# Performance work log

Hardware: AMD Instinct MI355X
Metric: run time of the kernel (lower is better)

The kernel has to match this reference:

```python
import jax, jax.numpy as jnp
import numpy as np

B, T, D, HS = 8, 2048, 768, 64
H = D // HS  # 12 heads
LN_EPS = 1e-5


def setup_inputs() -> dict:
    key = jax.random.key(0)
    ks = jax.random.split(key, 8)
    s = 0.02
    x = jax.random.normal(ks[0], (B, T, D), jnp.float32)
    Wx = jax.random.normal(ks[1], (D, D), jnp.float32) * s
    Ww = jax.random.normal(ks[2], (D, D), jnp.float32) * 0.01  # w_proj.weight ~ N(0,0.01)
    # w_proj bias schedule: logit(1 - linspace(0.9,0.999,H)) per head, expanded over head_size
    r_sched = jnp.linspace(0.9, 0.999, H)
    w_target = 1.0 - r_sched
    bw = jnp.log(w_target / (1.0 - w_target))          # logit
    bw = jnp.repeat(bw[:, None], HS, axis=1).reshape(-1)  # (D,)
    Wk = jax.random.normal(ks[3], (D, D), jnp.float32) * s
    Wv = jax.random.normal(ks[4], (D, D), jnp.float32) * s
    Wr = jax.random.normal(ks[5], (D, D), jnp.float32) * s
    Wo = jax.random.normal(ks[6], (D, D), jnp.float32) * s
    gamma = jnp.ones((D,), jnp.float32)
    beta = jnp.zeros((D,), jnp.float32)
    return {"x": x, "Wx": Wx, "Ww": Ww, "bw": bw, "Wk": Wk, "Wv": Wv,
            "Wr": Wr, "Wo": Wo, "gamma": gamma, "beta": beta}


def _layernorm(x, gamma, beta):
    mu = jnp.mean(x, axis=-1, keepdims=True)
    var = jnp.mean(jnp.square(x - mu), axis=-1, keepdims=True)
    return (x - mu) * jax.lax.rsqrt(var + LN_EPS) * gamma + beta


def _selective_scan(k, v, w):
    """k,v,w: (T,B,H,HS). State S: (B,H,HS,HS).
    S_t = (1 - w_t) * S_{t-1} (decay along key dim) + k_t (x) v_t;  y_t = k_t . S_t."""
    S0 = jnp.zeros((B, H, HS, HS), k.dtype)

    def step(S, inp):
        kt, vt, wt = inp  # each (B,H,HS)
        S = S * (1.0 - wt)[..., :, None] + kt[..., :, None] * vt[..., None, :]
        yt = jnp.einsum('bhi,bhij->bhj', kt, S)
        return S, yt

    _, ys = jax.lax.scan(step, S0, (k, v, w))
    return ys  # (T,B,H,HS)


def reference(x, Wx, Ww, bw, Wk, Wv, Wr, Wo, gamma, beta):
    xn = _layernorm(x, gamma, beta)                       # (B,T,D)
    xp = jnp.einsum('btd,ed->bte', xn, Wx)                # x_proj
    w = jax.nn.sigmoid(jnp.einsum('bte,fe->btf', xp, Ww) + bw)
    k = jnp.einsum('btd,ed->bte', xn, Wk)
    v = jnp.einsum('btd,ed->bte', xn, Wv)
    r = jax.nn.sigmoid(jnp.einsum('btd,ed->bte', xn, Wr))

    def to_scan(a):  # (B,T,D) -> (T,B,H,HS)
        return a.reshape(B, T, H, HS).transpose(1, 0, 2, 3)

    ys = _selective_scan(to_scan(k), to_scan(v), to_scan(w))  # (T,B,H,HS)
    y = ys.transpose(1, 0, 2, 3).reshape(B, T, D)
    y = y * r
    return jnp.einsum('btd,ed->bte', y, Wo)
```

## Files before the change

kernel.cpp:

```cpp
#include <hip/hip_runtime.h>

#define B_ 8
#define T_ 2048
#define D_ 768
#define H_ 12
#define HS_ 64
#define LN_EPS 1e-5f
#define NC 32
#define TC 64
#define PA 72
#define PV 68

typedef __attribute__((ext_vector_type(8))) short bf16x8;
typedef __attribute__((ext_vector_type(4))) float f32x4;

__device__ __forceinline__ ushort f2bf(float f) {
  unsigned u = __builtin_bit_cast(unsigned, f);
  unsigned r = (u + 0x7FFFu + ((u >> 16) & 1u)) >> 16;
  return (ushort)r;
}
__device__ __forceinline__ float bf2f(ushort u) {
  return __builtin_bit_cast(float, ((unsigned)u) << 16);
}

__device__ __forceinline__ bf16x8 ldsT68(const ushort* tile, int r0, int col) {
  bf16x8 r;
#pragma unroll
  for (int e = 0; e < 8; ++e) r[e] = (short)tile[(r0 + e) * PV + col];
  return r;
}

__global__ __launch_bounds__(256) void zero_out_kernel(float* __restrict__ out, int n) {
  for (int i = blockIdx.x * 256 + threadIdx.x; i < n; i += gridDim.x * 256)
    out[i] = 0.f;
}

__global__ __launch_bounds__(256) void cast_w_kernel(
    const float* __restrict__ src, ushort* __restrict__ dst) {
  int idx = (blockIdx.x * 256 + threadIdx.x) * 4;
  float4 v = *reinterpret_cast<const float4*>(src + idx);
  ushort4 o;
  o.x = f2bf(v.x); o.y = f2bf(v.y); o.z = f2bf(v.z); o.w = f2bf(v.w);
  *reinterpret_cast<ushort4*>(dst + idx) = o;
}

__global__ __launch_bounds__(256) void ln_kernel(
    const float* __restrict__ x, const float* __restrict__ gamma,
    const float* __restrict__ beta, ushort* __restrict__ xn) {
  const int wv = threadIdx.x >> 6;
  const int lane = threadIdx.x & 63;
  const int row = blockIdx.x * 4 + wv;
  const float* xr = x + (size_t)row * D_;
  float4 a[3];
#pragma unroll
  for (int s = 0; s < 3; ++s)
    a[s] = *reinterpret_cast<const float4*>(xr + s * 256 + lane * 4);
  float sum = 0.f;
#pragma unroll
  for (int s = 0; s < 3; ++s) sum += a[s].x + a[s].y + a[s].z + a[s].w;
#pragma unroll
  for (int off = 32; off; off >>= 1) sum += __shfl_xor(sum, off);
  float mu = sum * (1.f / 768.f);
  float vs = 0.f;
#pragma unroll
  for (int s = 0; s < 3; ++s) {
    float dx = a[s].x - mu, dy = a[s].y - mu, dz = a[s].z - mu, dw = a[s].w - mu;
    vs += dx * dx + dy * dy + dz * dz + dw * dw;
  }
#pragma unroll
  for (int off = 32; off; off >>= 1) vs += __shfl_xor(vs, off);
  float rs = rsqrtf(vs * (1.f / 768.f) + LN_EPS);
  ushort* orow = xn + (size_t)row * D_;
#pragma unroll
  for (int s = 0; s < 3; ++s) {
    int col = s * 256 + lane * 4;
    float4 g = *reinterpret_cast<const float4*>(gamma + col);
    float4 bb = *reinterpret_cast<const float4*>(beta + col);
    ushort4 o;
    o.x = f2bf((a[s].x - mu) * rs * g.x + bb.x);
    o.y = f2bf((a[s].y - mu) * rs * g.y + bb.y);
    o.z = f2bf((a[s].z - mu) * rs * g.z + bb.z);
    o.w = f2bf((a[s].w - mu) * rs * g.w + bb.w);
    *reinterpret_cast<ushort4*>(orow + col) = o;
  }
}

__global__ __launch_bounds__(512, 2) void gemm256(
    const ushort* __restrict__ A, const ushort* __restrict__ W,
    float* __restrict__ Cf,
    ushort* __restrict__ d0, ushort* __restrict__ d1,
    ushort* __restrict__ d2, ushort* __restrict__ d3,
    const float* __restrict__ bias, int mode) {
  __shared__ __align__(16) ushort lds[65536];
  const int tid = threadIdx.x;
  const int wid = tid >> 6;
  const int lane = tid & 63;
  const int wr = wid >> 2, wc = wid & 3;
  const int fr = lane & 15, fq = lane >> 4;
  const int m0 = blockIdx.x * 256, n0 = blockIdx.y * 256;
  const int strow = tid >> 3;
  const int stblk = tid & 7;

  const int RA0 = wr * 8192;
  const int RA1 = 32768 + wr * 8192;
  const int RB0 = 16384 + (wc >> 1) * 8192 + (wc & 1) * 4096;
  const int RB1 = 49152 + (wc >> 1) * 8192 + (wc & 1) * 4096;

  f32x4 acc[8][4];
#pragma unroll
  for (int m = 0; m < 8; ++m)
#pragma unroll
    for (int n = 0; n < 4; ++n) acc[m][n] = (f32x4){0.f, 0.f, 0.f, 0.f};

#define STAGE_HALF(gb, grow0, kk0, roff)                                          \
  {                                                                               \
    _Pragma("unroll") for (int j = 0; j < 2; ++j) {                               \
      const int lr_ = j * 64 + strow;                                             \
      const int bs_ = stblk ^ (lr_ & 7);                                          \
      const ushort* s_ = (gb) + (size_t)((grow0) + lr_) * 768 + (kk0) + bs_ * 8;  \
      __builtin_amdgcn_global_load_lds(                                           \
          (const __attribute__((address_space(1))) void*)s_,                      \
          (__attribute__((address_space(3))) void*)(lds + (roff) + j * 4096 + wid * 512), \
          16, 0, 0);                                                              \
    }                                                                             \
  }

#define LDF(dst, base, rf, kk)                                                    \
  dst = *reinterpret_cast<const bf16x8*>(                                         \
      lds + (base) + ((rf)*16 + fr) * 64 + ((((kk)*4 + fq) ^ (fr & 7)) * 8));

#define MFMA_Q(mb, nb, aa, bb)                                                    \
  __builtin_amdgcn_s_setprio(1);                                                  \
  _Pragma("unroll") for (int m_ = 0; m_ < 4; ++m_)                                \
  _Pragma("unroll") for (int n_ = 0; n_ < 2; ++n_)                                \
  _Pragma("unroll") for (int k_ = 0; k_ < 2; ++k_)                                \
    acc[(mb) + m_][(nb) + n_] = __builtin_amdgcn_mfma_f32_16x16x32_bf16(          \
        aa[m_][k_], bb[n_][k_], acc[(mb) + m_][(nb) + n_], 0, 0, 0);              \
  __builtin_amdgcn_s_setprio(0);

  STAGE_HALF(A, m0, 0, 0);
  STAGE_HALF(A, m0 + 128, 0, 8192);
  STAGE_HALF(W, n0, 0, 16384);
  STAGE_HALF(W, n0 + 128, 0, 24576);
  STAGE_HALF(W, n0, 64, 49152);
  STAGE_HALF(W, n0 + 128, 64, 57344);
  asm volatile("s_waitcnt vmcnt(4)" ::: "memory");
  __builtin_amdgcn_s_barrier();

  bf16x8 aL[4][2], aH[4][2], bL[2][2], bH[2][2];

  for (int i = 0; i < 6; ++i) {
    const int kQ = (2 * i + 1) * 64;
    const int kP2 = (2 * i + 2 <= 11 ? 2 * i + 2 : 11) * 64;
    const int kQ2 = (2 * i + 3 <= 11 ? 2 * i + 3 : 11) * 64;

    STAGE_HALF(A, m0, kQ, 32768);
#pragma unroll
    for (int m = 0; m < 4; ++m) { LDF(aL[m][0], RA0, m, 0); LDF(aL[m][1], RA0, m, 1); }
#pragma unroll
    for (int n = 0; n < 2; ++n) { LDF(bL[n][0], RB0, n, 0); LDF(bL[n][1], RB0, n, 1); }
    __builtin_amdgcn_s_barrier();
    MFMA_Q(0, 0, aL, bL);
    __builtin_amdgcn_s_barrier();
    STAGE_HALF(A, m0 + 128, kQ, 40960);
#pragma unroll
    for (int n = 0; n < 2; ++n) { LDF(bH[n][0], RB0, n + 2, 0); LDF(bH[n][1], RB0, n + 2, 1); }
    __builtin_amdgcn_s_barrier();
    MFMA_Q(0, 2, aL, bH);
    __builtin_amdgcn_s_barrier();
    STAGE_HALF(W, n0, kP2, 16384);
#pragma unroll
    for (int m = 0; m < 4; ++m) { LDF(aH[m][0], RA0, m + 4, 0); LDF(aH[m][1], RA0, m + 4, 1); }
    __builtin_amdgcn_s_barrier();
    MFMA_Q(4, 0, aH, bL);
    __builtin_amdgcn_s_barrier();
    STAGE_HALF(W, n0 + 128, kP2, 24576);
    __builtin_amdgcn_s_barrier();
    MFMA_Q(4, 2, aH, bH);
    asm volatile("s_waitcnt vmcnt(4)" ::: "memory");
    __builtin_amdgcn_s_barrier();

    STAGE_HALF(A, m0, kP2, 0);
#pragma unroll
    for (int m = 0; m < 4; ++m) { LDF(aL[m][0], RA1, m, 0); LDF(aL[m][1], RA1, m, 1); }
#pragma unroll
    for (int n = 0; n < 2; ++n) { LDF(bL[n][0], RB1, n, 0); LDF(bL[n][1], RB1, n, 1); }
    __builtin_amdgcn_s_barrier();
    MFMA_Q(0, 0, aL, bL);
    __builtin_amdgcn_s_barrier();
    STAGE_HALF(A, m0 + 128, kP2, 8192);
#pragma unroll
    for (int n = 0; n < 2; ++n) { LDF(bH[n][0], RB1, n + 2, 0); LDF(bH[n][1], RB1, n + 2, 1); }
    __builtin_amdgcn_s_barrier();
    MFMA_Q(0, 2, aL, bH);
    __builtin_amdgcn_s_barrier();
    STAGE_HALF(W, n0, kQ2, 49152);
#pragma unroll
    for (int m = 0; m < 4; ++m) { LDF(aH[m][0], RA1, m + 4, 0); LDF(aH[m][1], RA1, m + 4, 1); }
    __builtin_amdgcn_s_barrier();
    MFMA_Q(4, 0, aH, bL);
    __builtin_amdgcn_s_barrier();
    STAGE_HALF(W, n0 + 128, kQ2, 57344);
    __builtin_amdgcn_s_barrier();
    MFMA_Q(4, 2, aH, bH);
    asm volatile("s_waitcnt vmcnt(4)" ::: "memory");
    __builtin_amdgcn_s_barrier();
  }

  const int r0 = fq * 4;
  if (mode == 5) {
    const int sel = n0 >= 2304 ? 3 : n0 >= 1536 ? 2 : n0 >= 768 ? 1 : 0;
    ushort* dst = sel == 0 ? d0 : sel == 1 ? d1 : sel == 2 ? d2 : d3;
    const int nb = n0 - sel * 768;
    const bool sig = (sel == 2);
#pragma unroll
    for (int mf = 0; mf < 8; ++mf)
#pragma unroll
      for (int nf = 0; nf < 4; ++nf) {
        int gr = m0 + wr * 128 + mf * 16 + r0;
        int gc = nb + wc * 64 + nf * 16 + fr;
#pragma unroll
        for (int rr = 0; rr < 4; ++rr) {
          float v = acc[mf][nf][rr];
          if (sig) v = 1.f / (1.f + __expf(-v));
          dst[(size_t)(gr + rr) * 768 + gc] = f2bf(v);
        }
      }
  } else if (mode == 3) {
#pragma unroll
    for (int mf = 0; mf < 8; ++mf)
#pragma unroll
      for (int nf = 0; nf < 4; ++nf) {
        int gr = m0 + wr * 128 + mf * 16 + r0;
        int gc = n0 + wc * 64 + nf * 16 + fr;
        float bv = bias[gc];
#pragma unroll
        for (int rr = 0; rr < 4; ++rr) {
          float u = acc[mf][nf][rr] + bv;
          Cf[(size_t)(gr + rr) * 768 + gc] = 1.f / (1.f + __expf(u));
        }
      }
  } else {
#pragma unroll
    for (int mf = 0; mf < 8; ++mf)
#pragma unroll
      for (int nf = 0; nf < 4; ++nf) {
        int gr = m0 + wr * 128 + mf * 16 + r0;
        int gc = n0 + wc * 64 + nf * 16 + fr;
#pragma unroll
        for (int rr = 0; rr < 4; ++rr)
          Cf[(size_t)(gr + rr) * 768 + gc] = acc[mf][nf][rr];
      }
  }
#undef STAGE_HALF
#undef LDF
#undef MFMA_Q
}

__global__ __launch_bounds__(64) void scan_prep(
    const ushort* __restrict__ kb, const float* __restrict__ dg,
    ushort* __restrict__ kA, ushort* __restrict__ kIA, float* __restrict__ aend) {
  const int bh = blockIdx.x, c = blockIdx.y;
  const int b = bh / H_, h = bh % H_;
  const int i = threadIdx.x;
  size_t go = (size_t)b * T_ * D_ + (size_t)(c * TC) * D_ + h * HS_ + i;
  size_t co = ((size_t)bh * T_ + (size_t)c * TC) * HS_ + i;
  float a = 1.f;
#pragma unroll 4
  for (int t = 0; t < TC; ++t) {
    float d = dg[go];
    float k = bf2f(kb[go]);
    a *= d;
    kA[co] = f2bf(k * a);
    kIA[co] = f2bf(k / a);
    go += D_;
    co += HS_;
  }
  aend[((size_t)bh * NC + c) * HS_ + i] = a;
}

__global__ __launch_bounds__(256) void scan_mc(
    const ushort* __restrict__ kIA, const ushort* __restrict__ vb,
    char* __restrict__ McBase) {
  __shared__ __align__(16) ushort kt[TC * PV];
  __shared__ __align__(16) ushort vt[TC * PV];
  const int bh = blockIdx.x, c = blockIdx.y;
  const int b = bh / H_, h = bh % H_;
  const int tid = threadIdx.x;
  const int w = tid >> 6, lane = tid & 63;
  const int fr = lane & 15, fq = lane >> 4;
  {
    const int row = tid >> 2, col = (tid & 3) * 16;
    const ushort* gki = kIA + ((size_t)bh * T_ + (size_t)c * TC + row) * HS_ + col;
    const ushort* gv = vb + ((size_t)b * T_ + (size_t)c * TC + row) * D_ + h * HS_ + col;
    uint4 i0 = *(const uint4*)gki; uint4 i1 = *(const uint4*)(gki + 8);
    uint4 v0 = *(const uint4*)gv;  uint4 v1 = *(const uint4*)(gv + 8);
    ushort* pk = kt + row * PV + col;
    *(uint2*)(pk + 0) = make_uint2(i0.x, i0.y);
    *(uint2*)(pk + 4) = make_uint2(i0.z, i0.w);
    *(uint2*)(pk + 8) = make_uint2(i1.x, i1.y);
    *(uint2*)(pk + 12) = make_uint2(i1.z, i1.w);
    ushort* pv = vt + row * PV + col;
    *(uint2*)(pv + 0) = make_uint2(v0.x, v0.y);
    *(uint2*)(pv + 4) = make_uint2(v0.z, v0.w);
    *(uint2*)(pv + 8) = make_uint2(v1.x, v1.y);
    *(uint2*)(pv + 12) = make_uint2(v1.z, v1.w);
  }
  __syncthreads();
  f32x4 zero = {0.f, 0.f, 0.f, 0.f};
  f32x4 acc[4] = {zero, zero, zero, zero};
#pragma unroll
  for (int kk = 0; kk < 2; ++kk) {
    bf16x8 af = ldsT68(kt, kk * 32 + fq * 8, w * 16 + fr);
#pragma unroll
    for (int nf = 0; nf < 4; ++nf) {
      bf16x8 b8 = ldsT68(vt, kk * 32 + fq * 8, nf * 16 + fr);
      acc[nf] = __builtin_amdgcn_mfma_f32_16x16x32_bf16(af, b8, acc[nf], 0, 0, 0);
    }
  }
  float* mc = (float*)(McBase + ((size_t)bh * NC + c) * 16384);
#pragma unroll
  for (int nf = 0; nf < 4; ++nf)
#pragma unroll
    for (int rr = 0; rr < 4; ++rr) {
      int i = w * 16 + fq * 4 + rr, j = nf * 16 + fr;
      mc[i * 64 + j] = acc[nf][rr];
    }
}

__global__ __launch_bounds__(256) void scan_chain(
    char* __restrict__ McBase, const float* __restrict__ aend) {
  const int bh = blockIdx.x;
  const int i = threadIdx.x >> 2, j0 = (threadIdx.x & 3) * 16;
  float S[16];
#pragma unroll
  for (int p = 0; p < 16; ++p) S[p] = 0.f;
  for (int c = 0; c < NC; ++c) {
    char* slot = McBase + ((size_t)bh * NC + c) * 16384;
    const float* mc = (const float*)slot + i * 64 + j0;
    float m[16];
#pragma unroll
    for (int p = 0; p < 16; ++p) m[p] = mc[p];
    __syncthreads();
    ushort* s0 = (ushort*)slot + i * 64 + j0;
#pragma unroll
    for (int p = 0; p < 16; ++p) s0[p] = f2bf(S[p]);
    float ae = aend[((size_t)bh * NC + c) * HS_ + i];
#pragma unroll
    for (int p = 0; p < 16; ++p) S[p] = ae * (S[p] + m[p]);
  }
}

__global__ __launch_bounds__(256) void scan_y(
    const ushort* __restrict__ kA, const ushort* __restrict__ kIA,
    const ushort* __restrict__ vb, const ushort* __restrict__ rb,
    const char* __restrict__ McBase, ushort* __restrict__ yrow) {
  __shared__ __align__(16) ushort kAt[TC * PA];
  __shared__ __align__(16) ushort kIAt[TC * PA];
  __shared__ __align__(16) ushort Vt[TC * PV];
  __shared__ __align__(16) ushort S0t[TC * PV];
  __shared__ __align__(16) ushort Am[TC * PA];
  const int bh = blockIdx.x, c = blockIdx.y;
  const int b = bh / H_, h = bh % H_;
  const int tid = threadIdx.x;
  const int w = tid >> 6, lane = tid & 63;
  const int fr = lane & 15, fq = lane >> 4;
  {
    const int row = tid >> 2, col = (tid & 3) * 16;
    const ushort* gka = kA + ((size_t)bh * T_ + (size_t)c * TC + row) * HS_ + col;
    const ushort* gki = kIA + ((size_t)bh * T_ + (size_t)c * TC + row) * HS_ + col;
    const ushort* gv = vb + ((size_t)b * T_ + (size_t)c * TC + row) * D_ + h * HS_ + col;
    const ushort* gs = (const ushort*)(McBase + ((size_t)bh * NC + c) * 16384) + row * HS_ + col;
    uint4 a0 = *(const uint4*)gka; uint4 a1 = *(const uint4*)(gka + 8);
    uint4 i0 = *(const uint4*)gki; uint4 i1 = *(const uint4*)(gki + 8);
    uint4 v0 = *(const uint4*)gv;  uint4 v1 = *(const uint4*)(gv + 8);
    uint4 s0 = *(const uint4*)gs;  uint4 s1 = *(const uint4*)(gs + 8);
    *(uint4*)&kAt[row * PA + col] = a0;
    *(uint4*)&kAt[row * PA + col + 8] = a1;
    *(uint4*)&kIAt[row * PA + col] = i0;
    *(uint4*)&kIAt[row * PA + col + 8] = i1;
    ushort* pv = Vt + row * PV + col;
    *(uint2*)(pv + 0) = make_uint2(v0.x, v0.y);
    *(uint2*)(pv + 4) = make_uint2(v0.z, v0.w);
    *(uint2*)(pv + 8) = make_uint2(v1.x, v1.y);
    *(uint2*)(pv + 12) = make_uint2(v1.z, v1.w);
    ushort* ps = S0t + row * PV + col;
    *(uint2*)(ps + 0) = make_uint2(s0.x, s0.y);
    *(uint2*)(ps + 4) = make_uint2(s0.z, s0.w);
    *(uint2*)(ps + 8) = make_uint2(s1.x, s1.y);
    *(uint2*)(ps + 12) = make_uint2(s1.z, s1.w);
  }
  __syncthreads();

  f32x4 zero = {0.f, 0.f, 0.f, 0.f};
  {
    f32x4 accA[4] = {zero, zero, zero, zero};
#pragma unroll
    for (int kk = 0; kk < 2; ++kk) {
      bf16x8 af = *reinterpret_cast<const bf16x8*>(&kAt[(w * 16 + fr) * PA + kk * 32 + fq * 8]);
#pragma unroll
      for (int nf = 0; nf < 4; ++nf) {
        bf16x8 b8 = *reinterpret_cast<const bf16x8*>(&kIAt[(nf * 16 + fr) * PA + kk * 32 + fq * 8]);
        accA[nf] = __builtin_amdgcn_mfma_f32_16x16x32_bf16(af, b8, accA[nf], 0, 0, 0);
      }
    }
#pragma unroll
    for (int nf = 0; nf < 4; ++nf)
#pragma unroll
      for (int rr = 0; rr < 4; ++rr) {
        int t = w * 16 + fq * 4 + rr;
        int s = nf * 16 + fr;
        float val = (s <= t) ? accA[nf][rr] : 0.f;
        Am[t * PA + s] = f2bf(val);
      }
  }
  __syncthreads();

  f32x4 accY[4] = {zero, zero, zero, zero};
#pragma unroll
  for (int kk = 0; kk < 2; ++kk) {
    bf16x8 af = *reinterpret_cast<const bf16x8*>(&kAt[(w * 16 + fr) * PA + kk * 32 + fq * 8]);
#pragma unroll
    for (int nf = 0; nf < 4; ++nf) {
      bf16x8 b8 = ldsT68(S0t, kk * 32 + fq * 8, nf * 16 + fr);
      accY[nf] = __builtin_amdgcn_mfma_f32_16x16x32_bf16(af, b8, accY[nf], 0, 0, 0);
    }
  }
#pragma unroll
  for (int kk = 0; kk < 2; ++kk) {
    bf16x8 af = *reinterpret_cast<const bf16x8*>(&Am[(w * 16 + fr) * PA + kk * 32 + fq * 8]);
#pragma unroll
    for (int nf = 0; nf < 4; ++nf) {
      bf16x8 b8 = ldsT68(Vt, kk * 32 + fq * 8, nf * 16 + fr);
      accY[nf] = __builtin_amdgcn_mfma_f32_16x16x32_bf16(af, b8, accY[nf], 0, 0, 0);
    }
  }
#pragma unroll
  for (int nf = 0; nf < 4; ++nf)
#pragma unroll
    for (int rr = 0; rr < 4; ++rr) {
      int t = w * 16 + fq * 4 + rr;
      int j = nf * 16 + fr;
      size_t go = ((size_t)b * T_ + (size_t)c * TC + t) * D_ + h * HS_ + j;
      float rv = bf2f(rb[go]);
      yrow[go] = f2bf(accY[nf][rr] * rv);
    }
}

extern "C" void kernel_launch(void* const* d_in, const int* in_sizes, int n_in,
                              void* d_out, int out_size, void* d_ws, size_t ws_size,
                              hipStream_t stream) {
  const float* x     = (const float*)d_in[0];
  const float* Wx    = (const float*)d_in[1];
  const float* Ww    = (const float*)d_in[2];
  const float* bw    = (const float*)d_in[3];
  const float* Wk    = (const float*)d_in[4];
  const float* Wv    = (const float*)d_in[5];
  const float* Wr    = (const float*)d_in[6];
  const float* Wo    = (const float*)d_in[7];
  const float* gamma = (const float*)d_in[8];
  const float* beta  = (const float*)d_in[9];
  float* out = (float*)d_out;

  const size_t NEED = 208404480ull;
  if (ws_size < NEED) {
    zero_out_kernel<<<2048, 256, 0, stream>>>(out, out_size);
    return;
  }

  char* ws = (char*)d_ws;
  ushort* xn = (ushort*)ws;
  ushort* wb = (ushort*)(ws + 25165824);
  ushort* xp = (ushort*)(ws + 32243712);
  ushort* kb = (ushort*)(ws + 57409536);
  ushort* vb = (ushort*)(ws + 82575360);
  ushort* rb = (ushort*)(ws + 107741184);
  ushort* yr = (ushort*)(ws + 132907008);
  float*  df = (float*)(ws + 158072832);
  ushort* kAb  = (ushort*)ws;
  ushort* kIAb = (ushort*)(ws + 32243712);
  float*  aendb = (float*)(ws + 132907008);
  char*   McBase = (char*)(ws + 158072832);

  ushort* WcatB = wb;
  ushort* WwB = wb + 4 * 589824;
  ushort* WoB = wb + 5 * 589824;

  cast_w_kernel<<<576, 256, 0, stream>>>(Wk, WcatB);
  cast_w_kernel<<<576, 256, 0, stream>>>(Wv, WcatB + 589824);
  cast_w_kernel<<<576, 256, 0, stream>>>(Wr, WcatB + 2 * 589824);
  cast_w_kernel<<<576, 256, 0, stream>>>(Wx, WcatB + 3 * 589824);
  cast_w_kernel<<<576, 256, 0, stream>>>(Ww, WwB);
  cast_w_kernel<<<576, 256, 0, stream>>>(Wo, WoB);
  ln_kernel<<<4096, 256, 0, stream>>>(x, gamma, beta, xn);

  gemm256<<<dim3(64, 12), 512, 0, stream>>>(xn, WcatB, nullptr, kb, vb, rb, xp,
                                            nullptr, 5);
  gemm256<<<dim3(64, 3), 512, 0, stream>>>(xp, WwB, df, nullptr, nullptr, nullptr,
                                           nullptr, bw, 3);

  scan_prep<<<dim3(96, NC), 64, 0, stream>>>(kb, df, kAb, kIAb, aendb);
  scan_mc<<<dim3(96, NC), 256, 0, stream>>>(kIAb, vb, McBase);
  scan_chain<<<96, 256, 0, stream>>>(McBase, aendb);
  scan_y<<<dim3(96, NC), 256, 0, stream>>>(kAb, kIAb, vb, rb, McBase, yr);

  gemm256<<<dim3(64, 3), 512, 0, stream>>>(yr, WoB, out, nullptr, nullptr, nullptr,
                                           nullptr, nullptr, 0);
}
```

Measured before the change: 277.6 us.

## Fuse scan prep into chunk kernels, store V in MFMA fragment layout, pipeline GEMM LDS

```diff
diff --git a/kernel.cpp b/kernel.cpp
--- a/kernel.cpp
+++ b/kernel.cpp
@@ -8,8 +8,6 @@
 #define LN_EPS 1e-5f
 #define NC 32
 #define TC 64
-#define PA 72
-#define PV 68
 
 typedef __attribute__((ext_vector_type(8))) short bf16x8;
 typedef __attribute__((ext_vector_type(4))) float f32x4;
@@ -23,11 +21,11 @@
   return __builtin_bit_cast(float, ((unsigned)u) << 16);
 }
 
-__device__ __forceinline__ bf16x8 ldsT68(const ushort* tile, int r0, int col) {
-  bf16x8 r;
-#pragma unroll
-  for (int e = 0; e < 8; ++e) r[e] = (short)tile[(r0 + e) * PV + col];
-  return r;
+__device__ __forceinline__ int fragaddr(int t, int i) {
+  return ((t >> 4) * 2 + (i >> 5)) * 512 + ((((i >> 3) & 3) * 16) + (t & 15)) * 8 + (i & 7);
+}
+__device__ __forceinline__ int fragswz(int i) {
+  return (((i >> 3) & 3) << 3) ^ (((i >> 5) & 1) << 5);
 }
 
 __global__ __launch_bounds__(256) void zero_out_kernel(float* __restrict__ out, int n) {
@@ -138,6 +136,15 @@
         aa[m_][k_], bb[n_][k_], acc[(mb) + m_][(nb) + n_], 0, 0, 0);              \
   __builtin_amdgcn_s_setprio(0);
 
+#define LDF_AL(RA) \
+  _Pragma("unroll") for (int m = 0; m < 4; ++m) { LDF(aL[m][0], RA, m, 0); LDF(aL[m][1], RA, m, 1); }
+#define LDF_AH(RA) \
+  _Pragma("unroll") for (int m = 0; m < 4; ++m) { LDF(aH[m][0], RA, m + 4, 0); LDF(aH[m][1], RA, m + 4, 1); }
+#define LDF_BL(RB) \
+  _Pragma("unroll") for (int n = 0; n < 2; ++n) { LDF(bL[n][0], RB, n, 0); LDF(bL[n][1], RB, n, 1); }
+#define LDF_BH(RB) \
+  _Pragma("unroll") for (int n = 0; n < 2; ++n) { LDF(bH[n][0], RB, n + 2, 0); LDF(bH[n][1], RB, n + 2, 1); }
+
   STAGE_HALF(A, m0, 0, 0);
   STAGE_HALF(A, m0 + 128, 0, 8192);
   STAGE_HALF(W, n0, 0, 16384);
@@ -148,6 +155,8 @@
   __builtin_amdgcn_s_barrier();
 
   bf16x8 aL[4][2], aH[4][2], bL[2][2], bH[2][2];
+  LDF_AL(RA0);
+  LDF_BL(RB0);
 
   for (int i = 0; i < 6; ++i) {
     const int kQ = (2 * i + 1) * 64;
@@ -155,77 +164,95 @@
     const int kQ2 = (2 * i + 3 <= 11 ? 2 * i + 3 : 11) * 64;
 
     STAGE_HALF(A, m0, kQ, 32768);
-#pragma unroll
-    for (int m = 0; m < 4; ++m) { LDF(aL[m][0], RA0, m, 0); LDF(aL[m][1], RA0, m, 1); }
-#pragma unroll
-    for (int n = 0; n < 2; ++n) { LDF(bL[n][0], RB0, n, 0); LDF(bL[n][1], RB0, n, 1); }
+    LDF_BH(RB0);
     __builtin_amdgcn_s_barrier();
     MFMA_Q(0, 0, aL, bL);
     __builtin_amdgcn_s_barrier();
+
     STAGE_HALF(A, m0 + 128, kQ, 40960);
-#pragma unroll
-    for (int n = 0; n < 2; ++n) { LDF(bH[n][0], RB0, n + 2, 0); LDF(bH[n][1], RB0, n + 2, 1); }
+    LDF_AH(RA0);
     __builtin_amdgcn_s_barrier();
     MFMA_Q(0, 2, aL, bH);
     __builtin_amdgcn_s_barrier();
+
     STAGE_HALF(W, n0, kP2, 16384);
-#pragma unroll
-    for (int m = 0; m < 4; ++m) { LDF(aH[m][0], RA0, m + 4, 0); LDF(aH[m][1], RA0, m + 4, 1); }
     __builtin_amdgcn_s_barrier();
     MFMA_Q(4, 0, aH, bL);
     __builtin_amdgcn_s_barrier();
+
     STAGE_HALF(W, n0 + 128, kP2, 24576);
-    __builtin_amdgcn_s_barrier();
+    asm volatile("s_waitcnt vmcnt(4)" ::: "memory");
+    __builtin_amdgcn_s_barrier();
+    LDF_AL(RA1);
+    LDF_BL(RB1);
     MFMA_Q(4, 2, aH, bH);
+    __builtin_amdgcn_s_barrier();
+
+    STAGE_HALF(A, m0, kP2, 0);
+    LDF_BH(RB1);
+    __builtin_amdgcn_s_barrier();
+    MFMA_Q(0, 0, aL, bL);
+    __builtin_amdgcn_s_barrier();
+
+    STAGE_HALF(A, m0 + 128, kP2, 8192);
+    LDF_AH(RA1);
+    __builtin_amdgcn_s_barrier();
+    MFMA_Q(0, 2, aL, bH);
+    __builtin_amdgcn_s_barrier();
+
+    STAGE_HALF(W, n0, kQ2, 49152);
+    __builtin_amdgcn_s_barrier();
+    MFMA_Q(4, 0, aH, bL);
+    __builtin_amdgcn_s_barrier();
+
+    STAGE_HALF(W, n0 + 128, kQ2, 57344);
     asm volatile("s_waitcnt vmcnt(4)" ::: "memory");
     __builtin_amdgcn_s_barrier();
-
-    STAGE_HALF(A, m0, kP2, 0);
-#pragma unroll
-    for (int m = 0; m < 4; ++m) { LDF(aL[m][0], RA1, m, 0); LDF(aL[m][1], RA1, m, 1); }
-#pragma unroll
-    for (int n = 0; n < 2; ++n) { LDF(bL[n][0], RB1, n, 0); LDF(bL[n][1], RB1, n, 1); }
-    __builtin_amdgcn_s_barrier();
-    MFMA_Q(0, 0, aL, bL);
-    __builtin_amdgcn_s_barrier();
-    STAGE_HALF(A, m0 + 128, kP2, 8192);
-#pragma unroll
-    for (int n = 0; n < 2; ++n) { LDF(bH[n][0], RB1, n + 2, 0); LDF(bH[n][1], RB1, n + 2, 1); }
-    __builtin_amdgcn_s_barrier();
-    MFMA_Q(0, 2, aL, bH);
-    __builtin_amdgcn_s_barrier();
-    STAGE_HALF(W, n0, kQ2, 49152);
-#pragma unroll
-    for (int m = 0; m < 4; ++m) { LDF(aH[m][0], RA1, m + 4, 0); LDF(aH[m][1], RA1, m + 4, 1); }
-    __builtin_amdgcn_s_barrier();
-    MFMA_Q(4, 0, aH, bL);
-    __builtin_amdgcn_s_barrier();
-    STAGE_HALF(W, n0 + 128, kQ2, 57344);
-    __builtin_amdgcn_s_barrier();
+    LDF_AL(RA0);
+    LDF_BL(RB0);
     MFMA_Q(4, 2, aH, bH);
-    asm volatile("s_waitcnt vmcnt(4)" ::: "memory");
     __builtin_amdgcn_s_barrier();
   }
 
   const int r0 = fq * 4;
   if (mode == 5) {
     const int sel = n0 >= 2304 ? 3 : n0 >= 1536 ? 2 : n0 >= 768 ? 1 : 0;
-    ushort* dst = sel == 0 ? d0 : sel == 1 ? d1 : sel == 2 ? d2 : d3;
     const int nb = n0 - sel * 768;
-    const bool sig = (sel == 2);
-#pragma unroll
-    for (int mf = 0; mf < 8; ++mf)
-#pragma unroll
-      for (int nf = 0; nf < 4; ++nf) {
-        int gr = m0 + wr * 128 + mf * 16 + r0;
-        int gc = nb + wc * 64 + nf * 16 + fr;
-#pragma unroll
-        for (int rr = 0; rr < 4; ++rr) {
-          float v = acc[mf][nf][rr];
-          if (sig) v = 1.f / (1.f + __expf(-v));
-          dst[(size_t)(gr + rr) * 768 + gc] = f2bf(v);
+    if (sel == 1) {
+#pragma unroll
+      for (int mf = 0; mf < 8; ++mf)
+#pragma unroll
+        for (int nf = 0; nf < 4; ++nf) {
+          int gr = m0 + wr * 128 + mf * 16 + r0;
+          int gc = nb + wc * 64 + nf * 16 + fr;
+          int b = gr >> 11, t = gr & 2047;
+          int c = t >> 6, s0 = t & 63;
+          int h = gc >> 6, j = gc & 63;
+          size_t addr = ((size_t)((b * 12 + h) * 32 + c)) * 4096 +
+                        (size_t)(((j >> 4) * 2 + (s0 >> 5)) * 512 +
+                                 (((s0 >> 3) & 3) * 16 + (j & 15)) * 8 + (s0 & 7));
+          ushort4 o;
+          o.x = f2bf(acc[mf][nf][0]); o.y = f2bf(acc[mf][nf][1]);
+          o.z = f2bf(acc[mf][nf][2]); o.w = f2bf(acc[mf][nf][3]);
+          *reinterpret_cast<ushort4*>(d1 + addr) = o;
         }
-      }
+    } else {
+      ushort* dst = sel == 0 ? d0 : sel == 2 ? d2 : d3;
+      const bool sig = (sel == 2);
+#pragma unroll
+      for (int mf = 0; mf < 8; ++mf)
+#pragma unroll
+        for (int nf = 0; nf < 4; ++nf) {
+          int gr = m0 + wr * 128 + mf * 16 + r0;
+          int gc = nb + wc * 64 + nf * 16 + fr;
+#pragma unroll
+          for (int rr = 0; rr < 4; ++rr) {
+            float v = acc[mf][nf][rr];
+            if (sig) v = 1.f / (1.f + __expf(-v));
+            dst[(size_t)(gr + rr) * 768 + gc] = f2bf(v);
+          }
+        }
+    }
   } else if (mode == 3) {
 #pragma unroll
     for (int mf = 0; mf < 8; ++mf)
@@ -255,155 +282,183 @@
 #undef STAGE_HALF
 #undef LDF
 #undef MFMA_Q
-}
-
-__global__ __launch_bounds__(64) void scan_prep(
-    const ushort* __restrict__ kb, const float* __restrict__ dg,
-    ushort* __restrict__ kA, ushort* __restrict__ kIA, float* __restrict__ aend) {
+#undef LDF_AL
+#undef LDF_AH
+#undef LDF_BL
+#undef LDF_BH
+}
+
+__global__ __launch_bounds__(256) void scan_mc2(
+    const ushort* __restrict__ kb, const float* __restrict__ df,
+    const ushort* __restrict__ vbF, ushort* __restrict__ McT,
+    float* __restrict__ aend) {
+  __shared__ float dt[64 * 68];
+  __shared__ ushort kt[64 * 72];
+  __shared__ ushort kIAf[4096];
+  __shared__ float part[256];
   const int bh = blockIdx.x, c = blockIdx.y;
   const int b = bh / H_, h = bh % H_;
-  const int i = threadIdx.x;
-  size_t go = (size_t)b * T_ * D_ + (size_t)(c * TC) * D_ + h * HS_ + i;
-  size_t co = ((size_t)bh * T_ + (size_t)c * TC) * HS_ + i;
+  const int tid = threadIdx.x;
+  const int w = tid >> 6, lane = tid & 63;
+  {
+    const int row = tid >> 2, c16 = (tid & 3) * 16;
+    const ushort* gk = kb + ((size_t)(b * T_ + c * TC + row)) * D_ + h * HS_ + c16;
+    const float* gd = df + ((size_t)(b * T_ + c * TC + row)) * D_ + h * HS_ + c16;
+    uint4 k0 = *(const uint4*)gk;
+    uint4 k1 = *(const uint4*)(gk + 8);
+    *(uint4*)&kt[row * 72 + c16] = k0;
+    *(uint4*)&kt[row * 72 + c16 + 8] = k1;
+#pragma unroll
+    for (int q = 0; q < 4; ++q)
+      *(float4*)&dt[row * 68 + c16 + q * 4] = *(const float4*)(gd + q * 4);
+  }
+  __syncthreads();
+  float p = 1.f;
+#pragma unroll
+  for (int tt = 0; tt < 16; ++tt) p *= dt[(w * 16 + tt) * 68 + lane];
+  part[w * 64 + lane] = p;
+  __syncthreads();
   float a = 1.f;
-#pragma unroll 4
-  for (int t = 0; t < TC; ++t) {
-    float d = dg[go];
-    float k = bf2f(kb[go]);
+  for (int w2 = 0; w2 < w; ++w2) a *= part[w2 * 64 + lane];
+#pragma unroll
+  for (int tt = 0; tt < 16; ++tt) {
+    int t = w * 16 + tt;
+    float d = dt[t * 68 + lane];
+    float k = bf2f(kt[t * 72 + lane]);
     a *= d;
-    kA[co] = f2bf(k * a);
-    kIA[co] = f2bf(k / a);
-    go += D_;
-    co += HS_;
-  }
-  aend[((size_t)bh * NC + c) * HS_ + i] = a;
-}
-
-__global__ __launch_bounds__(256) void scan_mc(
-    const ushort* __restrict__ kIA, const ushort* __restrict__ vb,
-    char* __restrict__ McBase) {
-  __shared__ __align__(16) ushort kt[TC * PV];
-  __shared__ __align__(16) ushort vt[TC * PV];
+    kIAf[fragaddr(lane, t)] = f2bf(k / a);
+  }
+  if (w == 3) aend[((size_t)bh * NC + c) * 64 + lane] = a;
+  __syncthreads();
+
+  const int fr = lane & 15, fq = lane >> 4;
+  f32x4 acc[4];
+#pragma unroll
+  for (int nf = 0; nf < 4; ++nf) acc[nf] = (f32x4){0.f, 0.f, 0.f, 0.f};
+  bf16x8 af[2];
+  af[0] = *reinterpret_cast<const bf16x8*>(&kIAf[(w * 2 + 0) * 512 + lane * 8]);
+  af[1] = *reinterpret_cast<const bf16x8*>(&kIAf[(w * 2 + 1) * 512 + lane * 8]);
+  const ushort* vch = vbF + ((size_t)bh * NC + c) * 4096;
+#pragma unroll
+  for (int kk = 0; kk < 2; ++kk)
+#pragma unroll
+    for (int nf = 0; nf < 4; ++nf) {
+      bf16x8 b8 = *reinterpret_cast<const bf16x8*>(vch + (nf * 2 + kk) * 512 + lane * 8);
+      acc[nf] = __builtin_amdgcn_mfma_f32_16x16x32_bf16(af[kk], b8, acc[nf], 0, 0, 0);
+    }
+  ushort* mch = McT + ((size_t)bh * NC + c) * 4096;
+#pragma unroll
+  for (int nf = 0; nf < 4; ++nf) {
+    ushort4 o;
+    o.x = f2bf(acc[nf][0]); o.y = f2bf(acc[nf][1]);
+    o.z = f2bf(acc[nf][2]); o.w = f2bf(acc[nf][3]);
+    *reinterpret_cast<ushort4*>(&mch[(nf * 16 + fr) * 64 + w * 16 + fq * 4]) = o;
+  }
+}
+
+__global__ __launch_bounds__(256) void scan_chain2(
+    const ushort* __restrict__ McT, const float* __restrict__ aend,
+    ushort* __restrict__ S0F) {
+  const int bh = blockIdx.x;
+  const int j = threadIdx.x >> 2, i0 = (threadIdx.x & 3) * 16;
+  const int fbase = ((j >> 4) * 2 + (i0 >> 5)) * 512 + (((i0 >> 3) & 3) * 16 + (j & 15)) * 8;
+  float S[16];
+#pragma unroll
+  for (int p = 0; p < 16; ++p) S[p] = 0.f;
+  for (int c = 0; c < NC; ++c) {
+    const ushort* mch = McT + ((size_t)bh * NC + c) * 4096 + j * 64 + i0;
+    bf16x8 m0 = *reinterpret_cast<const bf16x8*>(mch);
+    bf16x8 m1 = *reinterpret_cast<const bf16x8*>(mch + 8);
+    const float* ae = aend + ((size_t)bh * NC + c) * 64 + i0;
+    float av[16];
+#pragma unroll
+    for (int q = 0; q < 4; ++q) {
+      float4 aq = *(const float4*)(ae + q * 4);
+      av[q * 4 + 0] = aq.x; av[q * 4 + 1] = aq.y; av[q * 4 + 2] = aq.z; av[q * 4 + 3] = aq.w;
+    }
+    ushort* s0 = S0F + ((size_t)bh * NC + c) * 4096 + fbase;
+    ushort4 o0, o1, o2, o3;
+    o0.x = f2bf(S[0]); o0.y = f2bf(S[1]); o0.z = f2bf(S[2]); o0.w = f2bf(S[3]);
+    o1.x = f2bf(S[4]); o1.y = f2bf(S[5]); o1.z = f2bf(S[6]); o1.w = f2bf(S[7]);
+    o2.x = f2bf(S[8]); o2.y = f2bf(S[9]); o2.z = f2bf(S[10]); o2.w = f2bf(S[11]);
+    o3.x = f2bf(S[12]); o3.y = f2bf(S[13]); o3.z = f2bf(S[14]); o3.w = f2bf(S[15]);
+    *reinterpret_cast<ushort4*>(s0) = o0;
+    *reinterpret_cast<ushort4*>(s0 + 4) = o1;
+    *reinterpret_cast<ushort4*>(s0 + 128) = o2;
+    *reinterpret_cast<ushort4*>(s0 + 132) = o3;
+#pragma unroll
+    for (int p = 0; p < 8; ++p) S[p] = av[p] * (S[p] + bf2f((ushort)m0[p]));
+#pragma unroll
+    for (int p = 0; p < 8; ++p) S[8 + p] = av[8 + p] * (S[8 + p] + bf2f((ushort)m1[p]));
+  }
+}
+
+__global__ __launch_bounds__(256) void scan_y2(
+    const ushort* __restrict__ kb, const float* __restrict__ df,
+    const ushort* __restrict__ vbF, const ushort* __restrict__ rb,
+    const ushort* __restrict__ S0F, ushort* __restrict__ yrow) {
+  __shared__ float dt[64 * 68];
+  __shared__ ushort kt[64 * 72];
+  __shared__ ushort kAf[4096];
+  __shared__ ushort kIAf[4096];
+  __shared__ ushort Am[64 * 72];
+  __shared__ float part[256];
   const int bh = blockIdx.x, c = blockIdx.y;
   const int b = bh / H_, h = bh % H_;
   const int tid = threadIdx.x;
   const int w = tid >> 6, lane = tid & 63;
   const int fr = lane & 15, fq = lane >> 4;
   {
-    const int row = tid >> 2, col = (tid & 3) * 16;
-    const ushort* gki = kIA + ((size_t)bh * T_ + (size_t)c * TC + row) * HS_ + col;
-    const ushort* gv = vb + ((size_t)b * T_ + (size_t)c * TC + row) * D_ + h * HS_ + col;
-    uint4 i0 = *(const uint4*)gki; uint4 i1 = *(const uint4*)(gki + 8);
-    uint4 v0 = *(const uint4*)gv;  uint4 v1 = *(const uint4*)(gv + 8);
-    ushort* pk = kt + row * PV + col;
-    *(uint2*)(pk + 0) = make_uint2(i0.x, i0.y);
-    *(uint2*)(pk + 4) = make_uint2(i0.z, i0.w);
-    *(uint2*)(pk + 8) = make_uint2(i1.x, i1.y);
-    *(uint2*)(pk + 12) = make_uint2(i1.z, i1.w);
-    ushort* pv = vt + row * PV + col;
-    *(uint2*)(pv + 0) = make_uint2(v0.x, v0.y);
-    *(uint2*)(pv + 4) = make_uint2(v0.z, v0.w);
-    *(uint2*)(pv + 8) = make_uint2(v1.x, v1.y);
-    *(uint2*)(pv + 12) = make_uint2(v1.z, v1.w);
-  }
-  __syncthreads();
-  f32x4 zero = {0.f, 0.f, 0.f, 0.f};
-  f32x4 acc[4] = {zero, zero, zero, zero};
+    const int row = tid >> 2, c16 = (tid & 3) * 16;
+    const ushort* gk = kb + ((size_t)(b * T_ + c * TC + row)) * D_ + h * HS_ + c16;
+    const float* gd = df + ((size_t)(b * T_ + c * TC + row)) * D_ + h * HS_ + c16;
+    uint4 k0 = *(const uint4*)gk;
+    uint4 k1 = *(const uint4*)(gk + 8);
+    *(uint4*)&kt[row * 72 + c16] = k0;
+    *(uint4*)&kt[row * 72 + c16 + 8] = k1;
+#pragma unroll
+    for (int q = 0; q < 4; ++q)
+      *(float4*)&dt[row * 68 + c16 + q * 4] = *(const float4*)(gd + q * 4);
+  }
+  __syncthreads();
+  float p = 1.f;
+#pragma unroll
+  for (int tt = 0; tt < 16; ++tt) p *= dt[(w * 16 + tt) * 68 + lane];
+  part[w * 64 + lane] = p;
+  __syncthreads();
+  float a = 1.f;
+  for (int w2 = 0; w2 < w; ++w2) a *= part[w2 * 64 + lane];
+  const int swz = fragswz(lane);
+#pragma unroll
+  for (int tt = 0; tt < 16; ++tt) {
+    int t = w * 16 + tt;
+    float d = dt[t * 68 + lane];
+    float k = bf2f(kt[t * 72 + lane]);
+    a *= d;
+    int ad = fragaddr(t, lane) ^ swz;
+    kAf[ad] = f2bf(k * a);
+    kIAf[ad] = f2bf(k / a);
+  }
+  __syncthreads();
+
+  bf16x8 af[2];
 #pragma unroll
   for (int kk = 0; kk < 2; ++kk) {
-    bf16x8 af = ldsT68(kt, kk * 32 + fq * 8, w * 16 + fr);
-#pragma unroll
-    for (int nf = 0; nf < 4; ++nf) {
-      bf16x8 b8 = ldsT68(vt, kk * 32 + fq * 8, nf * 16 + fr);
-      acc[nf] = __builtin_amdgcn_mfma_f32_16x16x32_bf16(af, b8, acc[nf], 0, 0, 0);
-    }
-  }
-  float* mc = (float*)(McBase + ((size_t)bh * NC + c) * 16384);
-#pragma unroll
-  for (int nf = 0; nf < 4; ++nf)
-#pragma unroll
-    for (int rr = 0; rr < 4; ++rr) {
-      int i = w * 16 + fq * 4 + rr, j = nf * 16 + fr;
-      mc[i * 64 + j] = acc[nf][rr];
-    }
-}
-
-__global__ __launch_bounds__(256) void scan_chain(
-    char* __restrict__ McBase, const float* __restrict__ aend) {
-  const int bh = blockIdx.x;
-  const int i = threadIdx.x >> 2, j0 = (threadIdx.x & 3) * 16;
-  float S[16];
-#pragma unroll
-  for (int p = 0; p < 16; ++p) S[p] = 0.f;
-  for (int c = 0; c < NC; ++c) {
-    char* slot = McBase + ((size_t)bh * NC + c) * 16384;
-    const float* mc = (const float*)slot + i * 64 + j0;
-    float m[16];
-#pragma unroll
-    for (int p = 0; p < 16; ++p) m[p] = mc[p];
-    __syncthreads();
-    ushort* s0 = (ushort*)slot + i * 64 + j0;
-#pragma unroll
-    for (int p = 0; p < 16; ++p) s0[p] = f2bf(S[p]);
-    float ae = aend[((size_t)bh * NC + c) * HS_ + i];
-#pragma unroll
-    for (int p = 0; p < 16; ++p) S[p] = ae * (S[p] + m[p]);
-  }
-}
-
-__global__ __launch_bounds__(256) void scan_y(
-    const ushort* __restrict__ kA, const ushort* __restrict__ kIA,
-    const ushort* __restrict__ vb, const ushort* __restrict__ rb,
-    const char* __restrict__ McBase, ushort* __restrict__ yrow) {
-  __shared__ __align__(16) ushort kAt[TC * PA];
-  __shared__ __align__(16) ushort kIAt[TC * PA];
-  __shared__ __align__(16) ushort Vt[TC * PV];
-  __shared__ __align__(16) ushort S0t[TC * PV];
-  __shared__ __align__(16) ushort Am[TC * PA];
-  const int bh = blockIdx.x, c = blockIdx.y;
-  const int b = bh / H_, h = bh % H_;
-  const int tid = threadIdx.x;
-  const int w = tid >> 6, lane = tid & 63;
-  const int fr = lane & 15, fq = lane >> 4;
+    int ra = ((w * 2 + kk) * 512 + lane * 8) ^ (((lane >> 4) << 3) ^ (kk << 5));
+    af[kk] = *reinterpret_cast<const bf16x8*>(&kAf[ra]);
+  }
   {
-    const int row = tid >> 2, col = (tid & 3) * 16;
-    const ushort* gka = kA + ((size_t)bh * T_ + (size_t)c * TC + row) * HS_ + col;
-    const ushort* gki = kIA + ((size_t)bh * T_ + (size_t)c * TC + row) * HS_ + col;
-    const ushort* gv = vb + ((size_t)b * T_ + (size_t)c * TC + row) * D_ + h * HS_ + col;
-    const ushort* gs = (const ushort*)(McBase + ((size_t)bh * NC + c) * 16384) + row * HS_ + col;
-    uint4 a0 = *(const uint4*)gka; uint4 a1 = *(const uint4*)(gka + 8);
-    uint4 i0 = *(const uint4*)gki; uint4 i1 = *(const uint4*)(gki + 8);
-    uint4 v0 = *(const uint4*)gv;  uint4 v1 = *(const uint4*)(gv + 8);
-    uint4 s0 = *(const uint4*)gs;  uint4 s1 = *(const uint4*)(gs + 8);
-    *(uint4*)&kAt[row * PA + col] = a0;
-    *(uint4*)&kAt[row * PA + col + 8] = a1;
-    *(uint4*)&kIAt[row * PA + col] = i0;
-    *(uint4*)&kIAt[row * PA + col + 8] = i1;
-    ushort* pv = Vt + row * PV + col;
-    *(uint2*)(pv + 0) = make_uint2(v0.x, v0.y);
-    *(uint2*)(pv + 4) = make_uint2(v0.z, v0.w);
-    *(uint2*)(pv + 8) = make_uint2(v1.x, v1.y);
-    *(uint2*)(pv + 12) = make_uint2(v1.z, v1.w);
-    ushort* ps = S0t + row * PV + col;
-    *(uint2*)(ps + 0) = make_uint2(s0.x, s0.y);
-    *(uint2*)(ps + 4) = make_uint2(s0.z, s0.w);
-    *(uint2*)(ps + 8) = make_uint2(s1.x, s1.y);
-    *(uint2*)(ps + 12) = make_uint2(s1.z, s1.w);
-  }
-  __syncthreads();
-
-  f32x4 zero = {0.f, 0.f, 0.f, 0.f};
-  {
-    f32x4 accA[4] = {zero, zero, zero, zero};
-#pragma unroll
-    for (int kk = 0; kk < 2; ++kk) {
-      bf16x8 af = *reinterpret_cast<const bf16x8*>(&kAt[(w * 16 + fr) * PA + kk * 32 + fq * 8]);
+    f32x4 accA[4];
+#pragma unroll
+    for (int nf = 0; nf < 4; ++nf) accA[nf] = (f32x4){0.f, 0.f, 0.f, 0.f};
+#pragma unroll
+    for (int kk = 0; kk < 2; ++kk)
 #pragma unroll
       for (int nf = 0; nf < 4; ++nf) {
-        bf16x8 b8 = *reinterpret_cast<const bf16x8*>(&kIAt[(nf * 16 + fr) * PA + kk * 32 + fq * 8]);
-        accA[nf] = __builtin_amdgcn_mfma_f32_16x16x32_bf16(af, b8, accA[nf], 0, 0, 0);
+        int rb8 = ((nf * 2 + kk) * 512 + lane * 8) ^ (((lane >> 4) << 3) ^ (kk << 5));
+        bf16x8 b8 = *reinterpret_cast<const bf16x8*>(&kIAf[rb8]);
+        accA[nf] = __builtin_amdgcn_mfma_f32_16x16x32_bf16(af[kk], b8, accA[nf], 0, 0, 0);
       }
-    }
 #pragma unroll
     for (int nf = 0; nf < 4; ++nf)
 #pragma unroll
@@ -411,28 +466,30 @@
         int t = w * 16 + fq * 4 + rr;
         int s = nf * 16 + fr;
         float val = (s <= t) ? accA[nf][rr] : 0.f;
-        Am[t * PA + s] = f2bf(val);
+        Am[t * 72 + s] = f2bf(val);
       }
   }
   __syncthreads();
 
-  f32x4 accY[4] = {zero, zero, zero, zero};
+  f32x4 accY[4];
+#pragma unroll
+  for (int nf = 0; nf < 4; ++nf) accY[nf] = (f32x4){0.f, 0.f, 0.f, 0.f};
+  const ushort* s0ch = S0F + ((size_t)bh * NC + c) * 4096;
+  const ushort* vch = vbF + ((size_t)bh * NC + c) * 4096;
+#pragma unroll
+  for (int kk = 0; kk < 2; ++kk)
+#pragma unroll
+    for (int nf = 0; nf < 4; ++nf) {
+      bf16x8 b8 = *reinterpret_cast<const bf16x8*>(s0ch + (nf * 2 + kk) * 512 + lane * 8);
+      accY[nf] = __builtin_amdgcn_mfma_f32_16x16x32_bf16(af[kk], b8, accY[nf], 0, 0, 0);
+    }
 #pragma unroll
   for (int kk = 0; kk < 2; ++kk) {
-    bf16x8 af = *reinterpret_cast<const bf16x8*>(&kAt[(w * 16 + fr) * PA + kk * 32 + fq * 8]);
+    bf16x8 am8 = *reinterpret_cast<const bf16x8*>(&Am[(w * 16 + fr) * 72 + kk * 32 + fq * 8]);
 #pragma unroll
     for (int nf = 0; nf < 4; ++nf) {
-      bf16x8 b8 = ldsT68(S0t, kk * 32 + fq * 8, nf * 16 + fr);
-      accY[nf] = __builtin_amdgcn_mfma_f32_16x16x32_bf16(af, b8, accY[nf], 0, 0, 0);
-    }
-  }
-#pragma unroll
-  for (int kk = 0; kk < 2; ++kk) {
-    bf16x8 af = *reinterpret_cast<const bf16x8*>(&Am[(w * 16 + fr) * PA + kk * 32 + fq * 8]);
-#pragma unroll
-    for (int nf = 0; nf < 4; ++nf) {
-      bf16x8 b8 = ldsT68(Vt, kk * 32 + fq * 8, nf * 16 + fr);
-      accY[nf] = __builtin_amdgcn_mfma_f32_16x16x32_bf16(af, b8, accY[nf], 0, 0, 0);
+      bf16x8 b8 = *reinterpret_cast<const bf16x8*>(vch + (nf * 2 + kk) * 512 + lane * 8);
+      accY[nf] = __builtin_amdgcn_mfma_f32_16x16x32_bf16(am8, b8, accY[nf], 0, 0, 0);
     }
   }
 #pragma unroll
@@ -473,14 +530,13 @@
   ushort* wb = (ushort*)(ws + 25165824);
   ushort* xp = (ushort*)(ws + 32243712);
   ushort* kb = (ushort*)(ws + 57409536);
-  ushort* vb = (ushort*)(ws + 82575360);
+  ushort* vbF = (ushort*)(ws + 82575360);
   ushort* rb = (ushort*)(ws + 107741184);
   ushort* yr = (ushort*)(ws + 132907008);
   float*  df = (float*)(ws + 158072832);
-  ushort* kAb  = (ushort*)ws;
-  ushort* kIAb = (ushort*)(ws + 32243712);
+  ushort* McT = (ushort*)ws;
+  ushort* S0F = (ushort*)(ws + 32243712);
   float*  aendb = (float*)(ws + 132907008);
-  char*   McBase = (char*)(ws + 158072832);
 
   ushort* WcatB = wb;
   ushort* WwB = wb + 4 * 589824;
@@ -494,15 +550,14 @@
   cast_w_kernel<<<576, 256, 0, stream>>>(Wo, WoB);
   ln_kernel<<<4096, 256, 0, stream>>>(x, gamma, beta, xn);
 
-  gemm256<<<dim3(64, 12), 512, 0, stream>>>(xn, WcatB, nullptr, kb, vb, rb, xp,
+  gemm256<<<dim3(64, 12), 512, 0, stream>>>(xn, WcatB, nullptr, kb, vbF, rb, xp,
                                             nullptr, 5);
   gemm256<<<dim3(64, 3), 512, 0, stream>>>(xp, WwB, df, nullptr, nullptr, nullptr,
                                            nullptr, bw, 3);
 
-  scan_prep<<<dim3(96, NC), 64, 0, stream>>>(kb, df, kAb, kIAb, aendb);
-  scan_mc<<<dim3(96, NC), 256, 0, stream>>>(kIAb, vb, McBase);
-  scan_chain<<<96, 256, 0, stream>>>(McBase, aendb);
-  scan_y<<<dim3(96, NC), 256, 0, stream>>>(kAb, kIAb, vb, rb, McBase, yr);
+  scan_mc2<<<dim3(96, NC), 256, 0, stream>>>(kb, df, vbF, McT, aendb);
+  scan_chain2<<<96, 256, 0, stream>>>(McT, aendb, S0F);
+  scan_y2<<<dim3(96, NC), 256, 0, stream>>>(kb, df, vbF, rb, S0F, yr);
 
   gemm256<<<dim3(64, 3), 512, 0, stream>>>(yr, WoB, out, nullptr, nullptr, nullptr,
                                            nullptr, nullptr, 0);
```

Result: slower. 432.6 us (+55.9%).
